# Performance work log

Measured on AMD Instinct MI355X. Metric: run time of the kernel, lower is better.

## Reference

```python
import jax, jax.numpy as jnp
import numpy as np
import math

B, S, D, NH = 2, 2048, 1024, 16
DK = D // NH
E, TOPK, MOE_H, NSH = 8, 2, 1024, 2
SH_H = MOE_H * NSH
EPS = 1e-6


def setup_inputs() -> dict:
    key = jax.random.key(0)
    ks = jax.random.split(key, 24)
    p = lambda k, shape: jax.random.normal(k, shape, jnp.float32) * 0.02
    x = jax.random.normal(ks[0], (B, S, D), jnp.float32)
    # RoPE tables: freqs_cis = exp(i * t * theta^{-2j/dk}), passed as cos/sin
    inv = 1.0 / (10000.0 ** (np.arange(0, DK, 2, dtype=np.float32) / DK))
    ang = np.outer(np.arange(S, dtype=np.float32), inv)
    freqs_cos = jnp.asarray(np.cos(ang), jnp.float32)
    freqs_sin = jnp.asarray(np.sin(ang), jnp.float32)
    mask = jnp.triu(jnp.full((S, S), -1e9, jnp.float32), k=1)  # causal additive mask
    return {
        'x': x, 'freqs_cos': freqs_cos, 'freqs_sin': freqs_sin, 'mask': mask,
        'wq': p(ks[1], (D, D)), 'wk': p(ks[2], (D, D)),
        'wv': p(ks[3], (D, D)), 'wo': p(ks[4], (D, D)),
        'attn_norm_w': jnp.ones((D,), jnp.float32),
        'ffn_norm_w': jnp.ones((D,), jnp.float32),
        'gate_w': p(ks[5], (E, D)), 'gate_b': p(ks[6], (E,)),
        'w1': p(ks[7], (E, MOE_H, D)), 'b1': p(ks[8], (E, MOE_H)),
        'w2': p(ks[9], (E, D, MOE_H)), 'b2': p(ks[10], (E, D)),
        'w3': p(ks[11], (E, MOE_H, D)), 'b3': p(ks[12], (E, MOE_H)),
        'sg_w': p(ks[13], (SH_H, D)), 'su_w': p(ks[14], (SH_H, D)),
        'sd_w': p(ks[15], (D, SH_H)),
    }


def rmsnorm(x, w):
    f = x.astype(jnp.float32)
    y = f * jax.lax.rsqrt(jnp.mean(f * f, axis=-1, keepdims=True) + EPS)
    return y.astype(x.dtype) * w


def rope(t, cos, sin):
    # t: [b, s, h, dk]; pairs (t[2j], t[2j+1]) as complex, multiplied by e^{i ang}
    tr, ti = t[..., 0::2], t[..., 1::2]
    c, s = cos[None, :, None, :], sin[None, :, None, :]
    outr = tr * c - ti * s
    outi = tr * s + ti * c
    return jnp.stack([outr, outi], axis=-1).reshape(t.shape)


def reference(x, freqs_cos, freqs_sin, mask, wq, wk, wv, wo, attn_norm_w, ffn_norm_w,
              gate_w, gate_b, w1, b1, w2, b2, w3, b3, sg_w, su_w, sd_w):
    b, s, d = x.shape
    # --- attention with RoPE ---
    h = rmsnorm(x, attn_norm_w)
    q = (h @ wq.T).reshape(b, s, NH, DK)
    k = (h @ wk.T).reshape(b, s, NH, DK)
    v = (h @ wv.T).reshape(b, s, NH, DK)
    q = rope(q, freqs_cos, freqs_sin)
    k = rope(k, freqs_cos, freqs_sin)
    scale = 1.0 / math.sqrt(DK)
    q = q.transpose(0, 2, 1, 3)
    k = k.transpose(0, 2, 1, 3)
    v = v.transpose(0, 2, 1, 3)
    scores = jnp.einsum('bhqd,bhkd->bhqk', q, k) * scale + mask
    # NOTE: source divides by sqrt(d_k) a second time before softmax (faithful quirk)
    attn = jax.nn.softmax(scores * scale, axis=-1)
    o = jnp.einsum('bhqk,bhkd->bhqd', attn, v).transpose(0, 2, 1, 3).reshape(b, s, d)
    x = x + o @ wo.T
    # --- MoE FFN ---
    hf = rmsnorm(x, ffn_norm_w).reshape(-1, d)                 # [T, D]
    gscores = jax.nn.softmax(hf @ gate_w.T + gate_b, axis=-1)  # [T, E]
    _, idx = jax.lax.top_k(gscores, TOPK)                      # bias is None -> topk on scores
    weights = jnp.take_along_axis(gscores, idx, axis=1)        # original_scores gather
    wmask = (jax.nn.one_hot(idx, E, dtype=hf.dtype) * weights[..., None]).sum(1)  # [T, E]
    shared = (jax.nn.silu(hf @ sg_w.T) * (hf @ su_w.T)) @ sd_w.T
    a1 = jnp.einsum('td,ehd->teh', hf, w1) + b1
    a3 = jnp.einsum('td,ehd->teh', hf, w3) + b3
    eo = jnp.einsum('teh,edh->ted', jax.nn.silu(a1) * a3, w2) + b2  # [T, E, D]
    router = jnp.einsum('te,ted->td', wmask, eo)
    return x + (shared + router).reshape(x.shape)
```

## Files before the change

### kernel.cpp

```cpp
#include <hip/hip_runtime.h>


typedef unsigned short u16;
typedef __attribute__((ext_vector_type(8))) short bh8;
typedef __attribute__((ext_vector_type(4))) float fv4;
typedef __attribute__((ext_vector_type(4))) unsigned uv4;
typedef __attribute__((ext_vector_type(2))) int iv2;

#define LOG2E 1.4426950408889634f
#define MAX_TILES 71

__device__ __forceinline__ float b2f(u16 u) {
  return __builtin_bit_cast(float, ((unsigned)u) << 16);
}
__device__ __forceinline__ u16 f2b(float f) {
  unsigned x = __builtin_bit_cast(unsigned, f);
  return (u16)((x + 0x7fffu + ((x >> 16) & 1u)) >> 16);
}
__device__ __forceinline__ fv4 mfma16(bh8 a, bh8 b, fv4 c) {
  return __builtin_amdgcn_mfma_f32_16x16x32_bf16(a, b, c, 0, 0, 0);
}
__device__ __forceinline__ unsigned cvtpk(float lo, float hi) {
  unsigned r;
  asm("v_cvt_pk_bf16_f32 %0, %1, %2" : "=v"(r) : "v"(lo), "v"(hi));
  return r;
}

__device__ __forceinline__ void xcd_swizzle(int& bx, int& by) {
  int gx = gridDim.x;
  int nwg = gx * gridDim.y;
  int flat = by * gx + bx;
  int q = nwg >> 3, r = nwg & 7;
  int xcd = flat & 7, idx = flat >> 3;
  int swz = (xcd < r ? xcd * (q + 1) : r * (q + 1) + (xcd - r) * q) + idx;
  by = swz / gx;
  bx = swz - by * gx;
}

#define GLD16(g, l)                                                        \
  __builtin_amdgcn_global_load_lds(                                        \
      (const __attribute__((address_space(1))) void*)(g),                  \
      (__attribute__((address_space(3))) void*)(l), 16, 0, 0)

__device__ __forceinline__ bh8 lds_frag(const u16* base, int row, int b8) {
  int off = row * 128 + ((b8 * 16) ^ ((row & 7) << 4));
  return *(const bh8*)((const char*)base + off);
}

template <int MODE, int TM = 128>
__global__ __launch_bounds__(256) void gemm_bt(
    const u16* __restrict__ A, const u16* __restrict__ B, int M, int N, int K,
    u16* __restrict__ Cb, float* __restrict__ Cf,
    const float* __restrict__ add1, const float* __restrict__ add2,
    const float* __restrict__ bias, const int* __restrict__ tmeta,
    const int* __restrict__ etok) {
  constexpr int MR = TM / 32;
  __shared__ u16 As[TM * 64];
  __shared__ u16 Bs[128 * 64];
  int bx = blockIdx.x, by = blockIdx.y;
  xcd_swizzle(bx, by);
  const int lane = threadIdx.x & 63;
  const int wid = threadIdx.x >> 6;
  const int wr = wid >> 1, wc = wid & 1;
  const int n0 = bx * 128;
  const int rr = lane >> 3;
  const int b8s = (lane & 7) ^ rr;
  const int ldA = (MODE == 6) ? M : K;

  int m0 = 0, e = 0, m0l = 0, cnt = 0, row0 = 0;
  const u16* Bp = B;
  if constexpr (MODE == 6 || MODE == 8) {
    int tile = by;
    if (tile >= tmeta[0]) return;
    e = tmeta[16 + tile * 4];
    m0l = tmeta[17 + tile * 4];
    cnt = tmeta[18 + tile * 4];
    row0 = tmeta[19 + tile * 4];
    Bp = B + (size_t)e * N * K;
  } else {
    m0 = by * TM;
  }

  const u16* Arow[MR];
  const u16* Brow[4];
#pragma unroll
  for (int i = 0; i < MR; ++i) {
    int c = wid * MR + i;
    int row = c * 8 + rr;
    if constexpr (MODE == 8) {
      int li = m0l + row;
      li = li < cnt ? li : cnt - 1;
      int tok = etok[e * 4096 + li];
      Arow[i] = A + (size_t)tok * ldA + b8s * 8;
    } else if constexpr (MODE == 6) {
      Arow[i] = A + (size_t)(row0 + row) * ldA + b8s * 8;
    } else {
      Arow[i] = A + (size_t)(m0 + row) * ldA + b8s * 8;
    }
  }
#pragma unroll
  for (int i = 0; i < 4; ++i)
    Brow[i] = Bp + (size_t)(n0 + (wid * 4 + i) * 8 + rr) * K + b8s * 8;

  fv4 acc[MR][4] = {};
  for (int k0 = 0; k0 < K; k0 += 64) {
    __syncthreads();
#pragma unroll
    for (int i = 0; i < MR; ++i)
      GLD16(Arow[i] + k0, &As[(wid * MR + i) * 512]);
#pragma unroll
    for (int i = 0; i < 4; ++i)
      GLD16(Brow[i] + k0, &Bs[(wid * 4 + i) * 512]);
    __syncthreads();
#pragma unroll
    for (int ks = 0; ks < 2; ++ks) {
      int b8 = ks * 4 + (lane >> 4);
      bh8 af[MR], bf[4];
#pragma unroll
      for (int mi = 0; mi < MR; ++mi)
        af[mi] = lds_frag(As, wr * (16 * MR) + mi * 16 + (lane & 15), b8);
#pragma unroll
      for (int ni = 0; ni < 4; ++ni)
        bf[ni] = lds_frag(Bs, wc * 64 + ni * 16 + (lane & 15), b8);
      __builtin_amdgcn_s_setprio(1);
#pragma unroll
      for (int mi = 0; mi < MR; ++mi)
#pragma unroll
        for (int ni = 0; ni < 4; ++ni)
          acc[mi][ni] = mfma16(af[mi], bf[ni], acc[mi][ni]);
      __builtin_amdgcn_s_setprio(0);
    }
  }

  const int rbase = (MODE == 6 || MODE == 8) ? row0 : m0;
  const int r0b = rbase + wr * (16 * MR) + (lane >> 4) * 4;
  const int c0b = n0 + wc * 64 + (lane & 15);

  if constexpr (MODE == 7 || MODE == 8) {
    const int OUTN = N >> 1;
    const int colb = (n0 >> 1) + wc * 32;
    const float* bb1 = nullptr;
    const float* bb3 = nullptr;
    if constexpr (MODE == 8) {
      bb1 = add1 + (size_t)e * OUTN;
      bb3 = add2 + (size_t)e * OUTN;
    }
#pragma unroll
    for (int mi = 0; mi < MR; ++mi) {
#pragma unroll
      for (int ni = 0; ni < 2; ++ni) {
        int c = colb + ni * 16 + (lane & 15);
#pragma unroll
        for (int r = 0; r < 4; ++r) {
          int row = r0b + mi * 16 + r;
          float xg = acc[mi][ni][r];
          float yu = acc[mi][ni + 2][r];
          if constexpr (MODE == 8) {
            xg += bb1[c];
            yu += bb3[c];
          }
          float s = xg / (1.f + __expf(-xg));
          Cb[(size_t)row * OUTN + c] = f2b(s * yu);
        }
      }
    }
  } else if constexpr (MODE == 9) {
#pragma unroll
    for (int mi = 0; mi < MR; ++mi) {
#pragma unroll
      for (int r = 0; r < 4; ++r) {
        int row = r0b + mi * 16 + r;
        int g0 = tmeta[2 * row], g1 = tmeta[2 * row + 1];
        float w0 = bias[2 * row], w1 = bias[2 * row + 1];
        const u16* e0p = Cb + (size_t)g0 * 1024;
        const u16* e1p = Cb + (size_t)g1 * 1024;
#pragma unroll
        for (int ni = 0; ni < 4; ++ni) {
          int c = c0b + ni * 16;
          size_t idx = (size_t)row * N + c;
          Cf[idx] = add1[idx] + acc[mi][ni][r] + w0 * b2f(e0p[c]) +
                    w1 * b2f(e1p[c]);
        }
      }
    }
  } else {
    const float* bb = nullptr;
    if constexpr (MODE == 6) bb = bias + (size_t)e * N;
#pragma unroll
    for (int mi = 0; mi < MR; ++mi) {
#pragma unroll
      for (int ni = 0; ni < 4; ++ni) {
        int c = c0b + ni * 16;
#pragma unroll
        for (int r = 0; r < 4; ++r) {
          int row = r0b + mi * 16 + r;
          size_t idx = (size_t)row * N + c;
          float v = acc[mi][ni][r];
          if constexpr (MODE == 0) Cb[idx] = f2b(v);
          else if constexpr (MODE == 1) Cf[idx] = add1[idx] + v;
          else Cb[idx] = f2b(v + bb[c]);
        }
      }
    }
  }
}

__global__ __launch_bounds__(256) void rmsnorm_bf16(
    const float* __restrict__ x, const float* __restrict__ w,
    u16* __restrict__ out) {
  int t = blockIdx.x;
  const float* xr = x + (size_t)t * 1024;
  fv4 v = *(const fv4*)(xr + threadIdx.x * 4);
  float ss = v[0] * v[0] + v[1] * v[1] + v[2] * v[2] + v[3] * v[3];
#pragma unroll
  for (int off = 1; off < 64; off <<= 1) ss += __shfl_xor(ss, off);
  __shared__ float red[4];
  int lane = threadIdx.x & 63, wid = threadIdx.x >> 6;
  if (lane == 0) red[wid] = ss;
  __syncthreads();
  float inv = rsqrtf((red[0] + red[1] + red[2] + red[3]) * (1.0f / 1024.f) + 1e-6f);
  u16* op = out + (size_t)t * 1024 + threadIdx.x * 4;
  const float* wp = w + threadIdx.x * 4;
#pragma unroll
  for (int i = 0; i < 4; ++i) op[i] = f2b(v[i] * inv * wp[i]);
}

__global__ __launch_bounds__(256) void rope_repack(
    const u16* __restrict__ qkv, const float* __restrict__ fc,
    const float* __restrict__ fs, u16* __restrict__ qr, u16* __restrict__ kr,
    u16* __restrict__ vt, int S) {
  __shared__ u16 tile[64][65];
  const int s0 = blockIdx.x * 64;
  const int b = blockIdx.y;
  const int h0 = blockIdx.z * 4;
#pragma unroll 4
  for (int it = 0; it < 32; ++it) {
    int idx = threadIdx.x + it * 256;
    int tl = idx >> 7, rem = idx & 127;
    int h = h0 + (rem >> 5), i = rem & 31;
    int s = s0 + tl;
    float c = fc[s * 32 + i], sn = fs[s * 32 + i];
    size_t src = ((size_t)(b * S + s)) * 3072 + h * 64 + 2 * i;
    size_t dst = ((size_t)((b * 16 + h) * S + s)) * 64 + 2 * i;
    float a0 = b2f(qkv[src]), a1 = b2f(qkv[src + 1]);
    qr[dst] = f2b(a0 * c - a1 * sn);
    qr[dst + 1] = f2b(a0 * sn + a1 * c);
    float b0 = b2f(qkv[src + 1024]), b1 = b2f(qkv[src + 1025]);
    kr[dst] = f2b(b0 * c - b1 * sn);
    kr[dst + 1] = f2b(b0 * sn + b1 * c);
  }
  for (int hh = 0; hh < 4; ++hh) {
    int h = h0 + hh;
    __syncthreads();
    for (int cc = threadIdx.x; cc < 512; cc += 256) {
      int tl = cc >> 3, d8 = cc & 7;
      bh8 val = *(const bh8*)(qkv + ((size_t)(b * S + s0 + tl)) * 3072 + 2048 +
                              h * 64 + d8 * 8);
#pragma unroll
      for (int j = 0; j < 8; ++j) tile[tl][d8 * 8 + j] = (u16)val[j];
    }
    __syncthreads();
    for (int cc = threadIdx.x; cc < 512; cc += 256) {
      int d = cc >> 3, pg = cc & 7;
      int sbase = 16 * (pg >> 2) + 4 * (pg & 3);
      bh8 o;
#pragma unroll
      for (int j = 0; j < 8; ++j)
        o[j] = (short)tile[sbase + (j & 3) + ((j >> 2) << 5)][d];
      *(bh8*)(vt + ((size_t)((b * 16 + h) * 64 + d)) * S + s0 + pg * 8) = o;
    }
  }
}

__global__ __launch_bounds__(256) void attn_fwd(
    const u16* __restrict__ qr, const u16* __restrict__ kr,
    const u16* __restrict__ vt, u16* __restrict__ ob, int S, int NHc) {
  __shared__ u16 Ks[2][64 * 64];
  __shared__ u16 Vs[2][64 * 64];
  const int lane = threadIdx.x & 63;
  const int wid = threadIdx.x >> 6;
  const int g = lane >> 4;
  const int l15 = lane & 15;
  const int bh = blockIdx.x;
  const int ia = blockIdx.y;
  const int nq = S / 64;
  const int qa0 = ia * 64;
  const int qb0 = (nq - 1 - ia) * 64;
  const int b = bh / NHc, h = bh % NHc;
  const u16* qbase = qr + (size_t)bh * S * 64;
  const u16* kb = kr + (size_t)bh * S * 64;
  const u16* vb = vt + (size_t)bh * 64 * S;
  const float SC = 0.015625f * LOG2E;
  const int rr = lane >> 3;
  const int b8s = (lane & 7) ^ rr;

  bh8 ONES;
#pragma unroll
  for (int j = 0; j < 8; ++j) ONES[j] = (short)0x3f80;

  bh8 qfA[2], qfB[2];
  {
    const u16* qp = qbase + (size_t)(qa0 + wid * 16 + l15) * 64 + g * 8;
    qfA[0] = *(const bh8*)qp;
    qfA[1] = *(const bh8*)(qp + 32);
    qp = qbase + (size_t)(qb0 + wid * 16 + l15) * 64 + g * 8;
    qfB[0] = *(const bh8*)qp;
    qfB[1] = *(const bh8*)(qp + 32);
  }
  fv4 oaccA[4] = {}, oaccB[4] = {};
  fv4 lA = {}, lB = {};
  float mA = -1e30f, mB = -1e30f;
  const int nktB = nq - ia;

  auto stage = [&](int buf, int j0) {
#pragma unroll
    for (int i = 0; i < 2; ++i) {
      int c = wid * 2 + i;
      int row = c * 8 + rr;
      GLD16(kb + (size_t)(j0 + row) * 64 + b8s * 8, &Ks[buf][c * 512]);
      GLD16(vb + (size_t)row * S + j0 + b8s * 8, &Vs[buf][c * 512]);
    }
  };
  stage(0, 0);

  auto process = [&](const bh8 (&kf)[2][4], const bh8 (&vf)[2][4], int j0,
                     int q0x, bh8* qf, fv4* oacc, float& mrow, fv4& lrowC) {
    const int q_my = q0x + wid * 16 + l15;
    fv4 st[4] = {};
    __builtin_amdgcn_s_setprio(1);
#pragma unroll
    for (int ks = 0; ks < 2; ++ks)
#pragma unroll
      for (int jt = 0; jt < 4; ++jt)
        st[jt] = mfma16(kf[ks][jt], qf[ks], st[jt]);
    __builtin_amdgcn_s_setprio(0);

    float sr[4][4];
    float mloc = -1e30f;
    const int jb = j0 + 4 * g;
    if (j0 + 63 > q0x + wid * 16) {
#pragma unroll
      for (int jt = 0; jt < 4; ++jt)
#pragma unroll
        for (int r = 0; r < 4; ++r) {
          int j = jb + jt * 16 + r;
          float s = (j <= q_my) ? st[jt][r] : -1e30f;
          sr[jt][r] = s;
          mloc = fmaxf(mloc, s);
        }
    } else {
#pragma unroll
      for (int jt = 0; jt < 4; ++jt)
#pragma unroll
        for (int r = 0; r < 4; ++r) {
          sr[jt][r] = st[jt][r];
          mloc = fmaxf(mloc, st[jt][r]);
        }
    }
    mloc = fmaxf(mloc, __shfl_xor(mloc, 16));
    mloc = fmaxf(mloc, __shfl_xor(mloc, 32));
    mloc *= SC;
    bool defer = __all(mloc <= mrow + 8.f);
    if (!defer) {
      float mnew = fmaxf(mrow, mloc);
      float sfac = exp2f(mrow - mnew);
      mrow = mnew;
      float sfC[4];
#pragma unroll
      for (int r = 0; r < 4; ++r) sfC[r] = __shfl(sfac, g * 4 + r);
#pragma unroll
      for (int dt = 0; dt < 4; ++dt)
#pragma unroll
        for (int r = 0; r < 4; ++r) oacc[dt][r] *= sfC[r];
#pragma unroll
      for (int r = 0; r < 4; ++r) lrowC[r] *= sfC[r];
    }
    float p[4][4];
#pragma unroll
    for (int jt = 0; jt < 4; ++jt)
#pragma unroll
      for (int r = 0; r < 4; ++r)
        p[jt][r] = exp2f(fmaf(sr[jt][r], SC, -mrow));

    __builtin_amdgcn_s_setprio(1);
    fv4 racc = {};
#pragma unroll
    for (int ks = 0; ks < 2; ++ks) {
      uv4 w;
      w[0] = cvtpk(p[ks][0], p[ks][1]);
      w[1] = cvtpk(p[ks][2], p[ks][3]);
      w[2] = cvtpk(p[ks + 2][0], p[ks + 2][1]);
      w[3] = cvtpk(p[ks + 2][2], p[ks + 2][3]);
      bh8 pa = __builtin_bit_cast(bh8, w);
      racc = mfma16(pa, ONES, racc);
#pragma unroll
      for (int dt = 0; dt < 4; ++dt)
        oacc[dt] = mfma16(pa, vf[ks][dt], oacc[dt]);
    }
    __builtin_amdgcn_s_setprio(0);
#pragma unroll
    for (int r = 0; r < 4; ++r) lrowC[r] += racc[r];
  };

  for (int kt = 0; kt < nktB; ++kt) {
    const int j0 = kt * 64;
    __syncthreads();
    if (kt + 1 < nktB) stage((kt + 1) & 1, (kt + 1) * 64);
    const u16* Kc = Ks[kt & 1];
    const u16* Vc = Vs[kt & 1];
    bh8 kf[2][4], vf[2][4];
#pragma unroll
    for (int ks = 0; ks < 2; ++ks) {
      int b8 = ks * 4 + g;
#pragma unroll
      for (int jt = 0; jt < 4; ++jt)
        kf[ks][jt] = lds_frag(Kc, jt * 16 + l15, b8);
#pragma unroll
      for (int dt = 0; dt < 4; ++dt)
        vf[ks][dt] = lds_frag(Vc, dt * 16 + l15, b8);
    }
    process(kf, vf, j0, qb0, qfB, oaccB, mB, lB);
    if (kt <= ia) process(kf, vf, j0, qa0, qfA, oaccA, mA, lA);
  }

  auto wout = [&](fv4* oacc, fv4 lrowC, int q0x) {
#pragma unroll
    for (int dt = 0; dt < 4; ++dt)
#pragma unroll
      for (int r = 0; r < 4; ++r) {
        int row = q0x + wid * 16 + g * 4 + r;
        int col = dt * 16 + l15;
        ob[((size_t)b * S + row) * 1024 + h * 64 + col] =
            f2b(oacc[dt][r] / lrowC[r]);
      }
  };
  wout(oaccA, lA, qa0);
  wout(oaccB, lB, qb0);
}

__global__ __launch_bounds__(256) void gate_topk(
    const float* __restrict__ x2, const float* __restrict__ nw,
    const float* __restrict__ gw, const float* __restrict__ gb,
    int* __restrict__ topk_e, float* __restrict__ topk_w,
    u16* __restrict__ hf) {
  int t = blockIdx.x * 4 + (threadIdx.x >> 6);
  int lane = threadIdx.x & 63;
  const float* xr = x2 + (size_t)t * 1024;
  float hv[16];
  float ss = 0.f;
#pragma unroll
  for (int i = 0; i < 4; ++i) {
    fv4 v = *(const fv4*)(xr + lane * 16 + i * 4);
#pragma unroll
    for (int j = 0; j < 4; ++j) {
      hv[i * 4 + j] = v[j];
      ss += v[j] * v[j];
    }
  }
#pragma unroll
  for (int off = 1; off < 64; off <<= 1) ss += __shfl_xor(ss, off);
  float inv = rsqrtf(ss * (1.0f / 1024.f) + 1e-6f);
  const fv4* nwp = (const fv4*)(nw + lane * 16);
#pragma unroll
  for (int i = 0; i < 4; ++i) {
    fv4 wv = nwp[i];
#pragma unroll
    for (int j = 0; j < 4; ++j) hv[i * 4 + j] *= inv * wv[j];
  }
  {
    bh8 o0, o1;
#pragma unroll
    for (int j = 0; j < 8; ++j) {
      o0[j] = (short)f2b(hv[j]);
      o1[j] = (short)f2b(hv[8 + j]);
    }
    u16* hp = hf + (size_t)t * 1024 + lane * 16;
    *(bh8*)hp = o0;
    *(bh8*)(hp + 8) = o1;
  }
  float logit[8];
#pragma unroll
  for (int e = 0; e < 8; ++e) {
    const fv4* wp = (const fv4*)(gw + (size_t)e * 1024 + lane * 16);
    float s = 0.f;
#pragma unroll
    for (int i = 0; i < 4; ++i) {
      fv4 wv = wp[i];
#pragma unroll
      for (int j = 0; j < 4; ++j) s += hv[i * 4 + j] * wv[j];
    }
    logit[e] = s;
  }
#pragma unroll
  for (int off = 1; off < 64; off <<= 1)
#pragma unroll
    for (int e = 0; e < 8; ++e) logit[e] += __shfl_xor(logit[e], off);
  if (lane == 0) {
#pragma unroll
    for (int e = 0; e < 8; ++e) logit[e] += gb[e];
    float mx = logit[0];
#pragma unroll
    for (int e = 1; e < 8; ++e) mx = fmaxf(mx, logit[e]);
    float pe[8], se = 0.f;
#pragma unroll
    for (int e = 0; e < 8; ++e) { pe[e] = __expf(logit[e] - mx); se += pe[e]; }
    float rs = 1.f / se;
#pragma unroll
    for (int e = 0; e < 8; ++e) pe[e] *= rs;
    int i0 = 0;
    float b0 = pe[0];
#pragma unroll
    for (int e = 1; e < 8; ++e)
      if (pe[e] > b0) { b0 = pe[e]; i0 = e; }
    int i1 = -1;
    float b1v = -1.f;
#pragma unroll
    for (int e = 0; e < 8; ++e)
      if (e != i0 && pe[e] > b1v) { b1v = pe[e]; i1 = e; }
    topk_e[2 * t] = i0;
    topk_e[2 * t + 1] = i1;
    topk_w[2 * t] = b0;
    topk_w[2 * t + 1] = b1v;
  }
}

__global__ __launch_bounds__(512) void route_tokens(
    const int* __restrict__ topk_e, int* __restrict__ pos_of,
    int* __restrict__ etok, int* __restrict__ meta, int* __restrict__ rowid,
    int T2) {
  __shared__ int scnt[8], sbase[8];
  const int e = threadIdx.x >> 6;
  const int lane = threadIdx.x & 63;
  int base = 0;
  for (int i0 = 0; i0 < T2; i0 += 128) {
    iv2 te = *(const iv2*)(topk_e + i0 + lane * 2);
    unsigned long long m0 = __ballot(te[0] == e);
    unsigned long long m1 = __ballot(te[1] == e);
    unsigned long long lt = (1ull << lane) - 1;
    int pre = __popcll(m0 & lt) + __popcll(m1 & lt);
    if (te[0] == e) {
      int pos = base + pre;
      etok[e * 4096 + pos] = (i0 >> 1) + lane;
      pos_of[i0 + lane * 2] = pos;
      ++pre;
    }
    if (te[1] == e) {
      int pos = base + pre;
      etok[e * 4096 + pos] = (i0 >> 1) + lane;
      pos_of[i0 + lane * 2 + 1] = pos;
    }
    base += __popcll(m0) + __popcll(m1);
  }
  if (lane == 0) scnt[e] = base;
  __syncthreads();
  if (threadIdx.x == 0) {
    int tt = 0, rb = 0;
#pragma unroll
    for (int e2 = 0; e2 < 8; ++e2) {
      sbase[e2] = rb;
      int c = scnt[e2];
      int nt = (c + 127) >> 7;
      for (int i = 0; i < nt; ++i) {
        meta[16 + tt * 4] = e2;
        meta[17 + tt * 4] = i * 128;
        meta[18 + tt * 4] = c;
        meta[19 + tt * 4] = rb + i * 128;
        ++tt;
      }
      rb += nt * 128;
    }
    meta[0] = tt;
  }
  __syncthreads();
  for (int i = threadIdx.x; i < T2; i += 512)
    rowid[i] = sbase[topk_e[i]] + pos_of[i];
}

__global__ __launch_bounds__(256) void f2b_convert(
    const float* __restrict__ src, u16* __restrict__ dst) {
  size_t i = ((size_t)blockIdx.x * 256 + threadIdx.x) * 8;
  fv4 a = *(const fv4*)(src + i);
  fv4 b = *(const fv4*)(src + i + 4);
  bh8 o;
#pragma unroll
  for (int j = 0; j < 4; ++j) o[j] = (short)f2b(a[j]);
#pragma unroll
  for (int j = 0; j < 4; ++j) o[4 + j] = (short)f2b(b[j]);
  *(bh8*)(dst + i) = o;
}

__global__ __launch_bounds__(256) void f2b_convert_ilv(
    const float* __restrict__ src, u16* __restrict__ dst, int half,
    int seg_shift) {
  size_t i = ((size_t)blockIdx.x * 256 + threadIdx.x) * 8;
  int r = (int)(i >> 10), col = (int)(i & 1023);
  int rl = r & ((1 << seg_shift) - 1), e = r >> seg_shift;
  int dstrow = (e << (seg_shift + 1)) + ((rl >> 5) << 6) + (rl & 31) +
               (half << 5);
  fv4 a = *(const fv4*)(src + i);
  fv4 b = *(const fv4*)(src + i + 4);
  bh8 o;
#pragma unroll
  for (int j = 0; j < 4; ++j) o[j] = (short)f2b(a[j]);
#pragma unroll
  for (int j = 0; j < 4; ++j) o[4 + j] = (short)f2b(b[j]);
  *(bh8*)(dst + (size_t)dstrow * 1024 + col) = o;
}

extern "C" void kernel_launch(void* const* d_in, const int* in_sizes, int n_in,
                              void* d_out, int out_size, void* d_ws,
                              size_t ws_size, hipStream_t stream) {
  (void)in_sizes; (void)n_in; (void)out_size; (void)ws_size;
  const int Sc = 2048, Dc = 1024, NHc = 16, Tc = 4096, SH = 2048;

  const float* x   = (const float*)d_in[0];
  const float* fc  = (const float*)d_in[1];
  const float* fs  = (const float*)d_in[2];
  const float* wq  = (const float*)d_in[4];
  const float* wk  = (const float*)d_in[5];
  const float* wv  = (const float*)d_in[6];
  const float* wo  = (const float*)d_in[7];
  const float* anw = (const float*)d_in[8];
  const float* fnw = (const float*)d_in[9];
  const float* gw  = (const float*)d_in[10];
  const float* gb  = (const float*)d_in[11];
  const float* w1  = (const float*)d_in[12];
  const float* b1  = (const float*)d_in[13];
  const float* w2  = (const float*)d_in[14];
  const float* b2  = (const float*)d_in[15];
  const float* w3  = (const float*)d_in[16];
  const float* b3  = (const float*)d_in[17];
  const float* sgw = (const float*)d_in[18];
  const float* suw = (const float*)d_in[19];
  const float* sdw = (const float*)d_in[20];
  float* out = (float*)d_out;

  char* base = (char*)d_ws;
  size_t off = 0;
  auto alloc = [&](size_t bytes) -> void* {
    void* p = base + off;
    off += (bytes + 255) & ~(size_t)255;
    return p;
  };
  u16* wqkv_b = (u16*)alloc(2ull * 3072 * 1024);
  u16* wo_b   = (u16*)alloc(2ull * 1024 * 1024);
  u16* sgu_b  = (u16*)alloc(2ull * 4096 * 1024);
  u16* sdw_b  = (u16*)alloc(2ull * 1024 * 2048);
  u16* w13_b  = (u16*)alloc(2ull * 8 * 2048 * 1024);
  u16* w2_b   = (u16*)alloc(2ull * 8 * 1024 * 1024);
  char* regA = (char*)alloc(2ull * Tc * 4096);
  char* regB = (char*)alloc(2ull * (size_t)MAX_TILES * 128 * 2048);
  float* x2  = (float*)alloc(4ull * Tc * Dc);
  u16* hs_b  = (u16*)alloc(2ull * Tc * SH);
  int* topk_e = (int*)alloc(2ull * Tc * 4);
  float* topk_w = (float*)alloc(2ull * Tc * 4);
  int* pos_of = (int*)alloc(2ull * Tc * 4);
  int* rowid = (int*)alloc(2ull * Tc * 4);
  int* etok = (int*)alloc(8ull * 4096 * 4);
  int* meta = (int*)alloc(512 * 4);

  u16* qkv_out = (u16*)regA;
  u16* eo_c    = (u16*)regA;
  u16* h_b  = (u16*)regB;
  u16* qr   = (u16*)regB;
  u16* kr   = (u16*)(regB + 2ull * Tc * Dc);
  u16* vt_  = (u16*)(regB + 4ull * Tc * Dc);
  u16* o_b  = (u16*)(regB + 6ull * Tc * Dc);
  u16* a13_c = (u16*)regB;
  u16* hf_b = wqkv_b;

  auto conv = [&](const float* s, u16* d, size_t n) {
    f2b_convert<<<dim3((unsigned)(n / 2048)), 256, 0, stream>>>(s, d);
  };
  conv(wq, wqkv_b, (size_t)Dc * Dc);
  conv(wk, wqkv_b + 1048576, (size_t)Dc * Dc);
  conv(wv, wqkv_b + 2097152, (size_t)Dc * Dc);
  conv(wo, wo_b, (size_t)Dc * Dc);
  conv(sdw, sdw_b, (size_t)Dc * SH);
  conv(w2, w2_b, 8ull * 1024 * 1024);
  f2b_convert_ilv<<<1024, 256, 0, stream>>>(sgw, sgu_b, 0, 11);
  f2b_convert_ilv<<<1024, 256, 0, stream>>>(suw, sgu_b, 1, 11);
  f2b_convert_ilv<<<4096, 256, 0, stream>>>(w1, w13_b, 0, 10);
  f2b_convert_ilv<<<4096, 256, 0, stream>>>(w3, w13_b, 1, 10);

  rmsnorm_bf16<<<Tc, 256, 0, stream>>>(x, anw, h_b);
  gemm_bt<0><<<dim3(3072 / 128, Tc / 128), 256, 0, stream>>>(
      h_b, wqkv_b, Tc, 3072, Dc, qkv_out, nullptr, nullptr, nullptr, nullptr,
      nullptr, nullptr);
  rope_repack<<<dim3(Sc / 64, 2, 4), 256, 0, stream>>>(qkv_out, fc, fs, qr, kr,
                                                       vt_, Sc);
  attn_fwd<<<dim3(2 * NHc, Sc / 128), 256, 0, stream>>>(qr, kr, vt_, o_b, Sc,
                                                        NHc);
  gemm_bt<1, 64><<<dim3(Dc / 128, Tc / 64), 256, 0, stream>>>(
      o_b, wo_b, Tc, Dc, Dc, nullptr, x2, x, nullptr, nullptr, nullptr,
      nullptr);

  gate_topk<<<Tc / 4, 256, 0, stream>>>(x2, fnw, gw, gb, topk_e, topk_w,
                                        hf_b);
  route_tokens<<<1, 512, 0, stream>>>(topk_e, pos_of, etok, meta, rowid,
                                      2 * Tc);

  gemm_bt<7><<<dim3(4096 / 128, Tc / 128), 256, 0, stream>>>(
      hf_b, sgu_b, Tc, 4096, Dc, hs_b, nullptr, nullptr, nullptr, nullptr,
      nullptr, nullptr);

  gemm_bt<8><<<dim3(2048 / 128, MAX_TILES), 256, 0, stream>>>(
      hf_b, w13_b, Tc, 2048, Dc, a13_c, nullptr, b1, b3, nullptr, meta, etok);
  gemm_bt<6><<<dim3(Dc / 128, MAX_TILES), 256, 0, stream>>>(
      a13_c, w2_b, 1024, Dc, 1024, eo_c, nullptr, nullptr, nullptr,
      b2, meta, etok);

  gemm_bt<9, 64><<<dim3(Dc / 128, Tc / 64), 256, 0, stream>>>(
      hs_b, sdw_b, Tc, Dc, SH, eo_c, out, x2, nullptr, topk_w, rowid,
      nullptr);
}
```

Before: 414.9 us.

## Double-buffer LDS tiles in GEMM to overlap global loads with MFMA

Turns the GEMM mainloop from a single-buffer load, sync, compute pattern into a double-buffered pipeline. Each iteration prefetches the next K-tile into the alternate LDS buffer with global_load_lds, then waits on vmcnt only for the current tile before computing. The aim is to hide global memory latency behind the MFMA work. In exchange it doubles the LDS footprint, which may lower occupancy, and relies on hand-set vmcnt counts and explicit barriers being correct.

```diff
diff --git a/kernel.cpp b/kernel.cpp
--- a/kernel.cpp
+++ b/kernel.cpp
@@ -55,8 +55,8 @@
     const float* __restrict__ bias, const int* __restrict__ tmeta,
     const int* __restrict__ etok) {
   constexpr int MR = TM / 32;
-  __shared__ u16 As[TM * 64];
-  __shared__ u16 Bs[128 * 64];
+  __shared__ u16 As[2][TM * 64];
+  __shared__ u16 Bs[2][128 * 64];
   int bx = blockIdx.x, by = blockIdx.y;
   xcd_swizzle(bx, by);
   const int lane = threadIdx.x & 63;
@@ -103,25 +103,45 @@
     Brow[i] = Bp + (size_t)(n0 + (wid * 4 + i) * 8 + rr) * K + b8s * 8;
 
   fv4 acc[MR][4] = {};
-  for (int k0 = 0; k0 < K; k0 += 64) {
-    __syncthreads();
-#pragma unroll
-    for (int i = 0; i < MR; ++i)
-      GLD16(Arow[i] + k0, &As[(wid * MR + i) * 512]);
-#pragma unroll
-    for (int i = 0; i < 4; ++i)
-      GLD16(Brow[i] + k0, &Bs[(wid * 4 + i) * 512]);
-    __syncthreads();
+  const int nt = K >> 6;
+
+#pragma unroll
+  for (int i = 0; i < MR; ++i)
+    GLD16(Arow[i], &As[0][(wid * MR + i) * 512]);
+#pragma unroll
+  for (int i = 0; i < 4; ++i)
+    GLD16(Brow[i], &Bs[0][(wid * 4 + i) * 512]);
+
+  for (int t = 0; t < nt; ++t) {
+    const int cur = t & 1;
+    if (t + 1 < nt) {
+      const int k0 = (t + 1) * 64;
+#pragma unroll
+      for (int i = 0; i < MR; ++i)
+        GLD16(Arow[i] + k0, &As[cur ^ 1][(wid * MR + i) * 512]);
+#pragma unroll
+      for (int i = 0; i < 4; ++i)
+        GLD16(Brow[i] + k0, &Bs[cur ^ 1][(wid * 4 + i) * 512]);
+      if constexpr (MR == 4)
+        asm volatile("s_waitcnt vmcnt(8)" ::: "memory");
+      else
+        asm volatile("s_waitcnt vmcnt(6)" ::: "memory");
+    } else {
+      asm volatile("s_waitcnt vmcnt(0)" ::: "memory");
+    }
+    __builtin_amdgcn_s_barrier();
+    __builtin_amdgcn_sched_barrier(0);
+
 #pragma unroll
     for (int ks = 0; ks < 2; ++ks) {
       int b8 = ks * 4 + (lane >> 4);
       bh8 af[MR], bf[4];
 #pragma unroll
       for (int mi = 0; mi < MR; ++mi)
-        af[mi] = lds_frag(As, wr * (16 * MR) + mi * 16 + (lane & 15), b8);
+        af[mi] = lds_frag(As[cur], wr * (16 * MR) + mi * 16 + (lane & 15), b8);
 #pragma unroll
       for (int ni = 0; ni < 4; ++ni)
-        bf[ni] = lds_frag(Bs, wc * 64 + ni * 16 + (lane & 15), b8);
+        bf[ni] = lds_frag(Bs[cur], wc * 64 + ni * 16 + (lane & 15), b8);
       __builtin_amdgcn_s_setprio(1);
 #pragma unroll
       for (int mi = 0; mi < MR; ++mi)
@@ -130,6 +150,9 @@
           acc[mi][ni] = mfma16(af[mi], bf[ni], acc[mi][ni]);
       __builtin_amdgcn_s_setprio(0);
     }
+    __builtin_amdgcn_sched_barrier(0);
+    __builtin_amdgcn_s_barrier();
+    __builtin_amdgcn_sched_barrier(0);
   }
 
   const int rbase = (MODE == 6 || MODE == 8) ? row0 : m0;
```

New measurement: 406.6 us. 1.02x faster.
